# Performance work log

Hardware: AMD Instinct MI355X
Metric: run time of the kernel (lower is better)

## Reference

```python
import jax, jax.numpy as jnp
import numpy as np

B, S, D_MODEL = 2, 2048, 2048
N_HEADS, N_KV = 32, 8
HEAD_DIM = D_MODEL // N_HEADS          # 64
HPG = N_HEADS // N_KV                  # heads per group = 4
DIM_K = HEAD_DIM * N_KV                # 512 (used as softmax scale per original code)


def setup_inputs() -> dict:
    key = jax.random.key(0)
    ks = jax.random.split(key, 11)
    s = lambda fan_in: 1.0 / np.sqrt(fan_in)
    return {
        "inputs_q": jax.random.normal(ks[0], (B, S, D_MODEL), jnp.float32),
        "inputs_k": jax.random.normal(ks[1], (B, S, D_MODEL), jnp.float32),
        "inputs_v": jax.random.normal(ks[2], (B, S, D_MODEL), jnp.float32),
        "Wq": jax.random.normal(ks[3], (D_MODEL, D_MODEL), jnp.float32) * s(D_MODEL),
        "bq": jnp.zeros((D_MODEL,), jnp.float32),
        "Wk": jax.random.normal(ks[4], (D_MODEL, DIM_K), jnp.float32) * s(D_MODEL),
        "bk": jnp.zeros((DIM_K,), jnp.float32),
        "Wv": jax.random.normal(ks[5], (D_MODEL, DIM_K), jnp.float32) * s(D_MODEL),
        "bv": jnp.zeros((DIM_K,), jnp.float32),
        "Wo": jax.random.normal(ks[6], (D_MODEL, D_MODEL), jnp.float32) * s(D_MODEL),
        "bo": jnp.zeros((D_MODEL,), jnp.float32),
    }


def reference(inputs_q, inputs_k, inputs_v, Wq, bq, Wk, bk, Wv, bv, Wo, bo):
    b, s, _ = inputs_q.shape
    q = inputs_q @ Wq + bq                       # [B,S,dim_q]
    k = inputs_k @ Wk + bk                       # [B,S,dim_k]
    v = inputs_v @ Wv + bv                       # [B,S,dim_v]
    q = q.reshape(b, s, N_KV, HPG, HEAD_DIM)     # b m g p d
    k = k.reshape(b, s, N_KV, HEAD_DIM)          # b n g d
    v = v.reshape(b, s, N_KV, HEAD_DIM)          # b n g d
    # logits[b,g,p,m,n] = q . k ; scale by sqrt(dim_k) per original code
    logits = jnp.einsum('bmgpd,bngd->bgpmn', q, k) / jnp.sqrt(jnp.float32(DIM_K))
    # causal mask (lower triangular allowed)
    causal = jnp.tril(jnp.ones((s, s), bool))
    logits = jnp.where(causal, logits, -jnp.inf)
    attn = jax.nn.softmax(logits, axis=-1)       # [B,G,P,M,N]
    out = jnp.einsum('bgpmn,bngd->bmgpd', attn, v)
    out = out.reshape(b, s, N_KV * HPG * HEAD_DIM)
    return out @ Wo + bo
```

## Files before the change

kernel.cpp:

```cpp
#include <hip/hip_runtime.h>
#include <hip/hip_bf16.h>

typedef __hip_bfloat16 bf16;
typedef float f32x4 __attribute__((ext_vector_type(4)));
typedef float f32x16 __attribute__((ext_vector_type(16)));
typedef short bf16x8 __attribute__((ext_vector_type(8)));

#define B_   2
#define S_   2048
#define DM   2048
#define HD   64
#define NH   32

__device__ __forceinline__ void async16(void* lds, const void* g) {
  __builtin_amdgcn_global_load_lds(
      (const __attribute__((address_space(1))) unsigned int*)g,
      (__attribute__((address_space(3))) unsigned int*)lds, 16, 0, 0);
}

__device__ __forceinline__ float exp2a(float x) {
  float r; asm("v_exp_f32 %0, %1" : "=v"(r) : "v"(x)); return r;
}
__device__ __forceinline__ unsigned cvtpk(float lo, float hi) {
  unsigned r; asm("v_cvt_pk_bf16_f32 %0, %1, %2" : "=v"(r) : "v"(lo), "v"(hi)); return r;
}
__device__ __forceinline__ void perm32swap(unsigned &a, unsigned &b) {
  asm volatile("v_permlane32_swap_b32 %0, %1" : "+v"(a), "+v"(b));
}

__global__ __launch_bounds__(256)
void prep_kernel(const float* __restrict__ xq, const float* __restrict__ xk,
                 const float* __restrict__ xv,
                 const float* __restrict__ Wq, const float* __restrict__ Wo,
                 const float* __restrict__ Wk, const float* __restrict__ Wv,
                 const float* __restrict__ bk, const float* __restrict__ bv,
                 bf16* __restrict__ Xq, bf16* __restrict__ Xk, bf16* __restrict__ Xv,
                 bf16* __restrict__ WqT, bf16* __restrict__ WoT, bf16* __restrict__ WkvT,
                 float* __restrict__ bkv) {
  const int blk = blockIdx.x;
  const int tid = threadIdx.x;

  if (blk < 12288) {
    const int a = blk >> 12;
    const int r = blk & 4095;
    const float* in = (a == 0) ? xq : (a == 1) ? xk : xv;
    bf16* out = (a == 0) ? Xq : (a == 1) ? Xk : Xv;
    const size_t i = ((size_t)r * 256 + tid) * 8;
    float4 v0 = *(const float4*)(in + i);
    float4 v1 = *(const float4*)(in + i + 4);
    union { bf16 h[8]; uint4 v; } u;
    u.h[0] = __float2bfloat16(v0.x); u.h[1] = __float2bfloat16(v0.y);
    u.h[2] = __float2bfloat16(v0.z); u.h[3] = __float2bfloat16(v0.w);
    u.h[4] = __float2bfloat16(v1.x); u.h[5] = __float2bfloat16(v1.y);
    u.h[6] = __float2bfloat16(v1.z); u.h[7] = __float2bfloat16(v1.w);
    *(uint4*)(out + i) = u.v;
    return;
  }

  int t = blk - 12288;
  const float* W; bf16* Wt; int N;
  if (t < 4096)       { W = Wq; Wt = WqT; N = 2048; }
  else if (t < 8192)  { t -= 4096; W = Wo; Wt = WoT; N = 2048; }
  else if (t < 9216)  { t -= 8192; W = Wk; Wt = WkvT; N = 512; }
  else if (t < 10240) { t -= 9216; W = Wv; Wt = WkvT + (size_t)512 * 2048; N = 512; }
  else {
    #pragma unroll
    for (int j = 0; j < 4; ++j) {
      const int i = tid * 4 + j;
      bkv[i] = (i < 512) ? bk[i] : bv[i - 512];
    }
    return;
  }
  const int k0 = (t & 63) * 32, n0 = (t >> 6) * 32;
  __shared__ float tile[32][33];
  const int tx = tid & 31, ty = tid >> 5;
  #pragma unroll
  for (int i = 0; i < 32; i += 8)
    tile[ty + i][tx] = W[(size_t)(k0 + ty + i) * N + n0 + tx];
  __syncthreads();
  #pragma unroll
  for (int i = 0; i < 32; i += 8)
    Wt[(size_t)(n0 + ty + i) * 2048 + k0 + tx] = __float2bfloat16(tile[tx][ty + i]);
}

__device__ __forceinline__ void store_out(float* C, size_t idx, float v) { C[idx] = v; }
__device__ __forceinline__ void store_out(bf16* C, size_t idx, float v) { C[idx] = __float2bfloat16(v); }

template <typename OUT>
__device__ __forceinline__ void gemm_body(const bf16* __restrict__ Au,
                                          const bf16* __restrict__ Bt,
                                          const float* __restrict__ bias, float omul,
                                          OUT* __restrict__ C, int N, int m0, int n0,
                                          bf16* As, bf16* Bs) {
  constexpr int BK = 32;
  const int tid = threadIdx.x;
  const int wave = tid >> 6, lane = tid & 63;
  const int l15 = lane & 15, l4 = lane >> 4;
  const int wm = (wave & 1) * 64, wn = (wave >> 1) * 64;

  f32x4 acc[4][4] = {};
  const int nk = 2048 / BK;

  auto stage = [&](int kt, int buf) {
    const int k0 = kt * BK;
    #pragma unroll
    for (int i = 0; i < 2; ++i) {
      const int rb = wave * 32 + i * 16;
      const int r  = rb + (lane >> 2);
      const int cs = (lane & 3) ^ ((r >> 1) & 3);
      async16(As + buf * 4096 + rb * BK, Au + (size_t)(m0 + r) * 2048 + k0 + cs * 8);
      async16(Bs + buf * 4096 + rb * BK, Bt + (size_t)(n0 + r) * 2048 + k0 + cs * 8);
    }
  };

  stage(0, 0);
  asm volatile("s_waitcnt vmcnt(0)" ::: "memory");
  __syncthreads();

  for (int kt = 0; kt < nk; ++kt) {
    const int cur = kt & 1;
    if (kt + 1 < nk) stage(kt + 1, cur ^ 1);
    bf16x8 af[4], bfr[4];
    #pragma unroll
    for (int f = 0; f < 4; ++f) {
      const int mr = wm + f * 16 + l15;
      af[f]  = *(const bf16x8*)(As + cur * 4096 + mr * BK + (l4 ^ ((mr >> 1) & 3)) * 8);
      const int nr = wn + f * 16 + l15;
      bfr[f] = *(const bf16x8*)(Bs + cur * 4096 + nr * BK + (l4 ^ ((nr >> 1) & 3)) * 8);
    }
    __builtin_amdgcn_s_setprio(1);
    #pragma unroll
    for (int i = 0; i < 4; ++i)
      #pragma unroll
      for (int j = 0; j < 4; ++j)
        acc[i][j] = __builtin_amdgcn_mfma_f32_16x16x32_bf16(af[i], bfr[j], acc[i][j], 0, 0, 0);
    __builtin_amdgcn_s_setprio(0);
    asm volatile("s_waitcnt vmcnt(0)" ::: "memory");
    __syncthreads();
  }

  const int r0 = m0 + wm + l4 * 4;
  const int c0 = n0 + wn + l15;
  #pragma unroll
  for (int j = 0; j < 4; ++j) {
    const int col = c0 + j * 16;
    const float bb = bias[col];
    #pragma unroll
    for (int i = 0; i < 4; ++i)
      #pragma unroll
      for (int r = 0; r < 4; ++r)
        store_out(C, (size_t)(r0 + i * 16 + r) * N + col, (acc[i][j][r] + bb) * omul);
  }
}

__global__ __launch_bounds__(256)
void gemm_qkv(const bf16* __restrict__ Xq, const bf16* __restrict__ Xk,
              const bf16* __restrict__ Xv,
              const bf16* __restrict__ WqT, const bf16* __restrict__ WkvT,
              const float* __restrict__ bq, const float* __restrict__ bkv,
              bf16* __restrict__ Qb, bf16* __restrict__ KVb) {
  __shared__ __align__(16) bf16 As[2][128 * 32];
  __shared__ __align__(16) bf16 Bs[2][128 * 32];
  const int bid = blockIdx.x;
  const int wg = (bid & 7) * 96 + (bid >> 3);
  if (wg < 512) {
    gemm_body<bf16>(Xq, WqT, bq, 0.063758717f, Qb, 2048,
                    (wg & 31) * 128, (wg >> 5) * 128, &As[0][0], &Bs[0][0]);
  } else {
    const int b2 = wg - 512;
    const int m0 = (b2 & 31) * 128, n0 = (b2 >> 5) * 128;
    gemm_body<bf16>(n0 < 512 ? Xk : Xv, WkvT, bkv, 1.0f, KVb, 1024,
                    m0, n0, &As[0][0], &Bs[0][0]);
  }
}

__global__ __launch_bounds__(256)
void gemm_o(const bf16* __restrict__ AO, const bf16* __restrict__ WoT,
            const float* __restrict__ bo, float* __restrict__ out) {
  __shared__ __align__(16) bf16 As[2][128 * 32];
  __shared__ __align__(16) bf16 Bs[2][128 * 32];
  gemm_body<float>(AO, WoT, bo, 1.0f, out, 2048,
                   blockIdx.x * 128, blockIdx.y * 128, &As[0][0], &Bs[0][0]);
}

__global__ __launch_bounds__(256, 3)
void attn_kernel(const bf16* __restrict__ Q, const bf16* __restrict__ KV, bf16* __restrict__ O) {
  const int pair = blockIdx.x, h = blockIdx.y, b = blockIdx.z;
  const int g = h >> 2;
  const int tid = threadIdx.x;
  const int wave = tid >> 6, lane = tid & 63;
  const int l31 = lane & 31, l5 = lane >> 5;

  __shared__ __align__(16) char smem[32768];
  bf16 (*Ks)[64 * 64] = (bf16(*)[64 * 64])smem;
  bf16 (*Vt)[64 * 64] = (bf16(*)[64 * 64])(smem + 16384);
  char* ob = smem + wave * 4608;

  const bf16* KVb = KV + (size_t)(b * S_) * 1024;
  const int kcol = g * HD;
  const int vcol = 512 + g * HD;
  const int kv2 = tid & 31, vd0 = (tid >> 5) * 8;

  for (int sub = 0; sub < 2; ++sub) {
    const int qt = (sub == 0) ? pair : 15 - pair;
    const int qbase = qt * 128;
    const int nt = 2 * qt + 2;
    const int qrow = qbase + wave * 32 + l31;
    const int wmax = qbase + wave * 32 + 31;

    bf16x8 qf[4];
    const bf16* qp = Q + (size_t)(b * S_ + qrow) * DM + h * HD + l5 * 8;
    #pragma unroll
    for (int ks = 0; ks < 4; ++ks) qf[ks] = *(const bf16x8*)(qp + ks * 16);

    f32x16 ot[2] = {};
    float m = -3.0e38f, lsum = 0.f;
    uint4 vr0, vr1;

    #pragma unroll
    for (int i2 = 0; i2 < 2; ++i2) {
      const int rb = wave * 16 + i2 * 8;
      const int r = rb + (lane >> 3);
      const int cs = (lane & 7) ^ (r & 7);
      async16(&Ks[0][rb * 64], KVb + (size_t)r * 1024 + kcol + cs * 8);
    }
    {
      const bf16* vp = KVb + (size_t)(2 * kv2) * 1024 + vcol + vd0;
      vr0 = *(const uint4*)vp;
      vr1 = *(const uint4*)(vp + 1024);
    }
    asm volatile("s_waitcnt vmcnt(0)" ::: "memory");
    {
      const unsigned short* a0 = (const unsigned short*)&vr0;
      const unsigned short* a1 = (const unsigned short*)&vr1;
      char* vb = (char*)Vt[0];
      #pragma unroll
      for (int j = 0; j < 8; ++j) {
        unsigned val = (unsigned)a0[j] | ((unsigned)a1[j] << 16);
        const int d = vd0 + j;
        *(unsigned*)(vb + d * 128 + ((kv2 * 4) ^ ((d & 7) << 4))) = val;
      }
    }
    __syncthreads();

    for (int t = 0; t < nt; ++t) {
      const int cur = t & 1;
      const int kv0 = t * 64;
      if (t + 1 < nt) {
        const int kvn = (t + 1) * 64;
        #pragma unroll
        for (int i2 = 0; i2 < 2; ++i2) {
          const int rb = wave * 16 + i2 * 8;
          const int r = rb + (lane >> 3);
          const int cs = (lane & 7) ^ (r & 7);
          async16(&Ks[cur ^ 1][rb * 64], KVb + (size_t)(kvn + r) * 1024 + kcol + cs * 8);
        }
        const bf16* vp = KVb + (size_t)(kvn + 2 * kv2) * 1024 + vcol + vd0;
        vr0 = *(const uint4*)vp;
        vr1 = *(const uint4*)(vp + 1024);
      }

      if (kv0 <= wmax) {
        f32x16 sT[2] = {};
        __builtin_amdgcn_s_setprio(1);
        #pragma unroll
        for (int ks = 0; ks < 4; ++ks) {
          #pragma unroll
          for (int i = 0; i < 2; ++i) {
            const int row = i * 32 + l31;
            bf16x8 kf = *(const bf16x8*)((const char*)Ks[cur] + row * 128 +
                                         ((ks * 32 + l5 * 16) ^ ((row & 7) << 4)));
            sT[i] = __builtin_amdgcn_mfma_f32_32x32x16_bf16(kf, qf[ks], sT[i], 0, 0, 0);
          }
        }
        __builtin_amdgcn_s_setprio(0);
        if (kv0 + 63 > qbase + wave * 32) {
          #pragma unroll
          for (int i = 0; i < 2; ++i)
            #pragma unroll
            for (int r = 0; r < 16; ++r) {
              const int kvg = kv0 + i * 32 + ((r & 3) + 8 * (r >> 2)) + 4 * l5;
              if (kvg > qrow) sT[i][r] = -3.0e38f;
            }
        }
        float a16[16];
        #pragma unroll
        for (int r = 0; r < 16; ++r) a16[r] = fmaxf(sT[0][r], sT[1][r]);
        #pragma unroll
        for (int s2 = 8; s2 >= 1; s2 >>= 1)
          #pragma unroll
          for (int r = 0; r < 8; ++r) if (r < s2) a16[r] = fmaxf(a16[r], a16[r + s2]);
        float pm = fmaxf(a16[0], __shfl_xor(a16[0], 32));
        if (!__all(pm - m <= 8.f)) {
          const float mn = fmaxf(m, pm);
          const float alpha = exp2a(m - mn);
          m = mn;
          lsum *= alpha;
          #pragma unroll
          for (int r = 0; r < 16; ++r) { ot[0][r] *= alpha; ot[1][r] *= alpha; }
        }
        float rs0 = 0.f, rs1 = 0.f;
        unsigned pk[2][8];
        #pragma unroll
        for (int i = 0; i < 2; ++i)
          #pragma unroll
          for (int rr = 0; rr < 8; ++rr) {
            const float p0 = exp2a(sT[i][2 * rr] - m);
            const float p1 = exp2a(sT[i][2 * rr + 1] - m);
            if (i == 0) rs0 += p0 + p1; else rs1 += p0 + p1;
            pk[i][rr] = cvtpk(p0, p1);
          }
        float rs = rs0 + rs1;
        rs += __shfl_xor(rs, 32);
        lsum += rs;
        #pragma unroll
        for (int i = 0; i < 2; ++i) {
          #pragma unroll
          for (int kp = 0; kp < 2; ++kp) {
            unsigned w0 = pk[i][4 * kp + 0], w1 = pk[i][4 * kp + 1];
            unsigned w2 = pk[i][4 * kp + 2], w3 = pk[i][4 * kp + 3];
            perm32swap(w0, w2);
            perm32swap(w1, w3);
            union { unsigned u[4]; bf16x8 v; } pf = {{w0, w1, w2, w3}};
            const int ks2 = i * 2 + kp;
            __builtin_amdgcn_s_setprio(1);
            #pragma unroll
            for (int f = 0; f < 2; ++f) {
              const int row = f * 32 + l31;
              bf16x8 vf = *(const bf16x8*)((const char*)Vt[cur] + row * 128 +
                                           ((ks2 * 32 + l5 * 16) ^ ((row & 7) << 4)));
              ot[f] = __builtin_amdgcn_mfma_f32_32x32x16_bf16(vf, pf.v, ot[f], 0, 0, 0);
            }
            __builtin_amdgcn_s_setprio(0);
          }
        }
      }

      asm volatile("s_waitcnt vmcnt(0)" ::: "memory");
      if (t + 1 < nt) {
        const unsigned short* a0 = (const unsigned short*)&vr0;
        const unsigned short* a1 = (const unsigned short*)&vr1;
        char* vb = (char*)Vt[cur ^ 1];
        #pragma unroll
        for (int j = 0; j < 8; ++j) {
          unsigned val = (unsigned)a0[j] | ((unsigned)a1[j] << 16);
          const int d = vd0 + j;
          *(unsigned*)(vb + d * 128 + ((kv2 * 4) ^ ((d & 7) << 4))) = val;
        }
      }
      __syncthreads();
    }

    const float inv = 1.0f / lsum;
    #pragma unroll
    for (int f = 0; f < 2; ++f)
      #pragma unroll
      for (int g2 = 0; g2 < 4; ++g2) {
        uint2 val;
        val.x = cvtpk(ot[f][g2 * 4 + 0] * inv, ot[f][g2 * 4 + 1] * inv);
        val.y = cvtpk(ot[f][g2 * 4 + 2] * inv, ot[f][g2 * 4 + 3] * inv);
        *(uint2*)(ob + l31 * 144 + f * 64 + g2 * 16 + l5 * 8) = val;
      }
    asm volatile("s_waitcnt lgkmcnt(0)" ::: "memory");
    __builtin_amdgcn_sched_barrier(0);
    #pragma unroll
    for (int rr = 0; rr < 4; ++rr) {
      const int row = rr * 8 + (lane >> 3);
      uint4 dv = *(const uint4*)(ob + row * 144 + (lane & 7) * 16);
      *(uint4*)(O + (size_t)(b * S_ + qbase + wave * 32 + row) * DM + h * HD + (lane & 7) * 8) = dv;
    }
    __syncthreads();
  }
}

extern "C" void kernel_launch(void* const* d_in, const int* in_sizes, int n_in,
                              void* d_out, int out_size, void* d_ws, size_t ws_size,
                              hipStream_t stream) {
  const float* xq = (const float*)d_in[0];
  const float* xk = (const float*)d_in[1];
  const float* xv = (const float*)d_in[2];
  const float* Wq = (const float*)d_in[3];
  const float* bq = (const float*)d_in[4];
  const float* Wk = (const float*)d_in[5];
  const float* bk = (const float*)d_in[6];
  const float* Wv = (const float*)d_in[7];
  const float* bv = (const float*)d_in[8];
  const float* Wo = (const float*)d_in[9];
  const float* bo = (const float*)d_in[10];
  float* out = (float*)d_out;

  char* ws = (char*)d_ws;
  bf16*  Xq   = (bf16*)(ws);
  bf16*  Xk   = (bf16*)(ws + 16777216);
  bf16*  Xv   = (bf16*)(ws + 33554432);
  bf16*  WqT  = (bf16*)(ws + 50331648);
  bf16*  WkvT = (bf16*)(ws + 58720256);
  bf16*  WoT  = (bf16*)(ws + 62914560);
  float* bkv  = (float*)(ws + 71303168);
  bf16*  Qb   = (bf16*)(ws + 71307264);
  bf16*  KVb  = (bf16*)(ws + 88084480);
  bf16*  AO   = Xq;

  prep_kernel<<<22529, 256, 0, stream>>>(xq, xk, xv, Wq, Wo, Wk, Wv, bk, bv,
                                         Xq, Xk, Xv, WqT, WoT, WkvT, bkv);
  gemm_qkv<<<768, 256, 0, stream>>>(Xq, Xk, Xv, WqT, WkvT, bq, bkv, Qb, KVb);
  attn_kernel<<<dim3(8, 32, 2), 256, 0, stream>>>(Qb, KVb, AO);
  gemm_o<<<dim3(32, 16), 256, 0, stream>>>(AO, WoT, bo, out);
}
```

Baseline: 236.7 us.

## Triple-buffer K tiles in attention and prefetch two tiles ahead

The attention kernel's K staging goes from double to triple buffering. Async global-to-LDS loads are now issued two KV tiles ahead, and targeted vmcnt waits replace full drains, so K loads can overlap more compute. V stays double-buffered through registers. The full __syncthreads is replaced with an explicit lgkmcnt wait plus s_barrier. LDS use grows from 32KB to 40KB per block, which could limit occupancy, and the vmcnt accounting depends on the exact order in which loads are issued.

```diff
diff --git a/kernel.cpp b/kernel.cpp
--- a/kernel.cpp
+++ b/kernel.cpp
@@ -16,6 +16,10 @@
   __builtin_amdgcn_global_load_lds(
       (const __attribute__((address_space(1))) unsigned int*)g,
       (__attribute__((address_space(3))) unsigned int*)lds, 16, 0, 0);
+}
+
+template <int N> __device__ __forceinline__ void waitvm() {
+  asm volatile("s_waitcnt vmcnt(%0)" :: "i"(N) : "memory");
 }
 
 __device__ __forceinline__ float exp2a(float x) {
@@ -191,15 +195,36 @@
   const int wave = tid >> 6, lane = tid & 63;
   const int l31 = lane & 31, l5 = lane >> 5;
 
-  __shared__ __align__(16) char smem[32768];
-  bf16 (*Ks)[64 * 64] = (bf16(*)[64 * 64])smem;
-  bf16 (*Vt)[64 * 64] = (bf16(*)[64 * 64])(smem + 16384);
+  __shared__ __align__(16) char smem[40960];
+  bf16* KsBuf = (bf16*)smem;
+  bf16* VtBuf = (bf16*)(smem + 24576);
   char* ob = smem + wave * 4608;
 
   const bf16* KVb = KV + (size_t)(b * S_) * 1024;
   const int kcol = g * HD;
   const int vcol = 512 + g * HD;
   const int kv2 = tid & 31, vd0 = (tid >> 5) * 8;
+
+  auto stageK = [&](int buf, int kv0) {
+    #pragma unroll
+    for (int i2 = 0; i2 < 2; ++i2) {
+      const int rb = wave * 16 + i2 * 8;
+      const int r = rb + (lane >> 3);
+      const int cs = (lane & 7) ^ (r & 7);
+      async16(KsBuf + buf * 4096 + rb * 64, KVb + (size_t)(kv0 + r) * 1024 + kcol + cs * 8);
+    }
+  };
+  auto writeV = [&](int buf, uint4 va, uint4 vb) {
+    const unsigned short* a0 = (const unsigned short*)&va;
+    const unsigned short* a1 = (const unsigned short*)&vb;
+    char* base = (char*)VtBuf + buf * 8192;
+    #pragma unroll
+    for (int j = 0; j < 8; ++j) {
+      unsigned val = (unsigned)a0[j] | ((unsigned)a1[j] << 16);
+      const int d = vd0 + j;
+      *(unsigned*)(base + d * 128 + ((kv2 * 4) ^ ((d & 7) << 4))) = val;
+    }
+  };
 
   for (int sub = 0; sub < 2; ++sub) {
     const int qt = (sub == 0) ? pair : 15 - pair;
@@ -217,50 +242,32 @@
     float m = -3.0e38f, lsum = 0.f;
     uint4 vr0, vr1;
 
-    #pragma unroll
-    for (int i2 = 0; i2 < 2; ++i2) {
-      const int rb = wave * 16 + i2 * 8;
-      const int r = rb + (lane >> 3);
-      const int cs = (lane & 7) ^ (r & 7);
-      async16(&Ks[0][rb * 64], KVb + (size_t)r * 1024 + kcol + cs * 8);
-    }
     {
       const bf16* vp = KVb + (size_t)(2 * kv2) * 1024 + vcol + vd0;
       vr0 = *(const uint4*)vp;
       vr1 = *(const uint4*)(vp + 1024);
     }
-    asm volatile("s_waitcnt vmcnt(0)" ::: "memory");
-    {
-      const unsigned short* a0 = (const unsigned short*)&vr0;
-      const unsigned short* a1 = (const unsigned short*)&vr1;
-      char* vb = (char*)Vt[0];
-      #pragma unroll
-      for (int j = 0; j < 8; ++j) {
-        unsigned val = (unsigned)a0[j] | ((unsigned)a1[j] << 16);
-        const int d = vd0 + j;
-        *(unsigned*)(vb + d * 128 + ((kv2 * 4) ^ ((d & 7) << 4))) = val;
-      }
-    }
-    __syncthreads();
+    stageK(0, 0);
+    stageK(1, 64);
+    waitvm<4>();
+    writeV(0, vr0, vr1);
+    waitvm<2>();
+    asm volatile("s_waitcnt lgkmcnt(0)" ::: "memory");
+    __builtin_amdgcn_s_barrier();
+    asm volatile("" ::: "memory");
 
     for (int t = 0; t < nt; ++t) {
-      const int cur = t & 1;
       const int kv0 = t * 64;
       if (t + 1 < nt) {
-        const int kvn = (t + 1) * 64;
-        #pragma unroll
-        for (int i2 = 0; i2 < 2; ++i2) {
-          const int rb = wave * 16 + i2 * 8;
-          const int r = rb + (lane >> 3);
-          const int cs = (lane & 7) ^ (r & 7);
-          async16(&Ks[cur ^ 1][rb * 64], KVb + (size_t)(kvn + r) * 1024 + kcol + cs * 8);
-        }
-        const bf16* vp = KVb + (size_t)(kvn + 2 * kv2) * 1024 + vcol + vd0;
+        const bf16* vp = KVb + (size_t)((t + 1) * 64 + 2 * kv2) * 1024 + vcol + vd0;
         vr0 = *(const uint4*)vp;
         vr1 = *(const uint4*)(vp + 1024);
       }
+      if (t + 2 < nt) stageK((t + 2) % 3, (t + 2) * 64);
 
       if (kv0 <= wmax) {
+        const char* kb = (const char*)(KsBuf + (t % 3) * 4096);
+        const char* vb = (const char*)(VtBuf + (t & 1) * 4096);
         f32x16 sT[2] = {};
         __builtin_amdgcn_s_setprio(1);
         #pragma unroll
@@ -268,7 +275,7 @@
           #pragma unroll
           for (int i = 0; i < 2; ++i) {
             const int row = i * 32 + l31;
-            bf16x8 kf = *(const bf16x8*)((const char*)Ks[cur] + row * 128 +
+            bf16x8 kf = *(const bf16x8*)(kb + row * 128 +
                                          ((ks * 32 + l5 * 16) ^ ((row & 7) << 4)));
             sT[i] = __builtin_amdgcn_mfma_f32_32x32x16_bf16(kf, qf[ks], sT[i], 0, 0, 0);
           }
@@ -327,7 +334,7 @@
             #pragma unroll
             for (int f = 0; f < 2; ++f) {
               const int row = f * 32 + l31;
-              bf16x8 vf = *(const bf16x8*)((const char*)Vt[cur] + row * 128 +
+              bf16x8 vf = *(const bf16x8*)(vb + row * 128 +
                                            ((ks2 * 32 + l5 * 16) ^ ((row & 7) << 4)));
               ot[f] = __builtin_amdgcn_mfma_f32_32x32x16_bf16(vf, pf.v, ot[f], 0, 0, 0);
             }
@@ -336,19 +343,12 @@
         }
       }
 
-      asm volatile("s_waitcnt vmcnt(0)" ::: "memory");
-      if (t + 1 < nt) {
-        const unsigned short* a0 = (const unsigned short*)&vr0;
-        const unsigned short* a1 = (const unsigned short*)&vr1;
-        char* vb = (char*)Vt[cur ^ 1];
-        #pragma unroll
-        for (int j = 0; j < 8; ++j) {
-          unsigned val = (unsigned)a0[j] | ((unsigned)a1[j] << 16);
-          const int d = vd0 + j;
-          *(unsigned*)(vb + d * 128 + ((kv2 * 4) ^ ((d & 7) << 4))) = val;
-        }
-      }
-      __syncthreads();
+      if (t + 2 < nt) waitvm<2>();
+      else            waitvm<0>();
+      if (t + 1 < nt) writeV((t + 1) & 1, vr0, vr1);
+      asm volatile("s_waitcnt lgkmcnt(0)" ::: "memory");
+      __builtin_amdgcn_s_barrier();
+      asm volatile("" ::: "memory");
     }
 
     const float inv = 1.0f / lsum;
```

Measured after the change: 231.9 us. 1.02x faster.
